# Performance work log

Measured on AMD Instinct MI355X. Metric: run time of the kernel, lower is better.

The kernel has to match this reference:

```python
import math
import jax, jax.numpy as jnp
import numpy as np

C = 1024
H = 16
HD = C // H
T = 2048
B = 2
EPS = 1e-5


def setup_inputs() -> dict:
    key = jax.random.key(0)
    ks = jax.random.split(key, 8)
    s = 0.02
    return {
        "x": jax.random.normal(ks[0], (B, T, C), dtype=jnp.float32),
        "ln1_g": jnp.ones((C,), jnp.float32),
        "ln1_b": jnp.zeros((C,), jnp.float32),
        "w_attn": jax.random.normal(ks[1], (C, 3 * C), dtype=jnp.float32) * s,
        "b_attn": jnp.zeros((3 * C,), jnp.float32),
        "w_proj": jax.random.normal(ks[2], (C, C), dtype=jnp.float32) * s,
        "b_proj": jnp.zeros((C,), jnp.float32),
        "ln2_g": jnp.ones((C,), jnp.float32),
        "ln2_b": jnp.zeros((C,), jnp.float32),
        "w_fc": jax.random.normal(ks[3], (C, 4 * C), dtype=jnp.float32) * s,
        "b_fc": jnp.zeros((4 * C,), jnp.float32),
        "w_fc2": jax.random.normal(ks[4], (4 * C, C), dtype=jnp.float32) * s,
        "b_fc2": jnp.zeros((C,), jnp.float32),
    }


def _layernorm(x, g, b):
    mu = jnp.mean(x, axis=-1, keepdims=True)
    var = jnp.mean((x - mu) ** 2, axis=-1, keepdims=True)
    return (x - mu) * jax.lax.rsqrt(var + EPS) * g + b


def _attention(x, w_attn, b_attn, w_proj, b_proj):
    Bb, Tt, Cc = x.shape
    qkv = x @ w_attn + b_attn  # (B,T,3C)
    q, k, v = jnp.split(qkv, 3, axis=-1)
    # (B,H,T,HD)
    q = q.reshape(Bb, Tt, H, HD).transpose(0, 2, 1, 3)
    k = k.reshape(Bb, Tt, H, HD).transpose(0, 2, 1, 3)
    v = v.reshape(Bb, Tt, H, HD).transpose(0, 2, 1, 3)
    scale = 1.0 / math.sqrt(HD)
    attn = jnp.einsum("bhqd,bhkd->bhqk", q, k) * scale
    causal = jnp.tril(jnp.ones((Tt, Tt), dtype=bool))
    attn = jnp.where(causal[None, None], attn, -jnp.inf)
    attn = jax.nn.softmax(attn, axis=-1)
    out = jnp.einsum("bhqk,bhkd->bhqd", attn, v)
    out = out.transpose(0, 2, 1, 3).reshape(Bb, Tt, Cc)
    return out @ w_proj + b_proj


def _mlp(x, w_fc, b_fc, w_fc2, b_fc2):
    h = jax.nn.gelu(x @ w_fc + b_fc, approximate=True)
    return h @ w_fc2 + b_fc2


def reference(x, ln1_g, ln1_b, w_attn, b_attn, w_proj, b_proj,
              ln2_g, ln2_b, w_fc, b_fc, w_fc2, b_fc2):
    x = x + _attention(_layernorm(x, ln1_g, ln1_b), w_attn, b_attn, w_proj, b_proj)
    x = x + _mlp(_layernorm(x, ln2_g, ln2_b), w_fc, b_fc, w_fc2, b_fc2)
    return x
```

## Files before the change

### kernel.cpp

```cpp
#include <hip/hip_runtime.h>
#include <math.h>

#define TB 2
#define TT 2048
#define TC 1024
#define TH 16
#define THD 64
#define TM (TB*TT)
#define NQT 32

typedef __bf16 bf16x8 __attribute__((ext_vector_type(8)));
typedef float f32x4 __attribute__((ext_vector_type(4)));
typedef unsigned short u16x8 __attribute__((ext_vector_type(8)));
typedef unsigned short u16x4 __attribute__((ext_vector_type(4)));

__device__ __forceinline__ unsigned short f2bf(float f){
    unsigned int u = __builtin_bit_cast(unsigned int, f);
    u = (u + 0x7FFFu + ((u >> 16) & 1u)) >> 16;
    return (unsigned short)u;
}
__device__ __forceinline__ float bf2f(unsigned short h){
    unsigned int u = ((unsigned int)h) << 16;
    return __builtin_bit_cast(float, u);
}
__device__ __forceinline__ bf16x8 ldbf8(const unsigned short* p){
    return __builtin_bit_cast(bf16x8, *(const u16x8*)p);
}
__device__ __forceinline__ void gl_lds16(const void* g, void* l){
    __builtin_amdgcn_global_load_lds(
        (const __attribute__((address_space(1))) unsigned int*)g,
        (__attribute__((address_space(3))) unsigned int*)l,
        16, 0, 0);
}
__device__ __forceinline__ float gelu_tanh(float v){
    float u = 2.0f * 0.7978845608028654f * (v + 0.044715f * v * v * v);
    u = fminf(fmaxf(u, -30.f), 30.f);
    float e = __expf(u);
    return 0.5f * v * (1.f + (e - 1.f) / (e + 1.f));
}

__global__ __launch_bounds__(256)
void convert_all(const float* __restrict__ w_attn, const float* __restrict__ w_proj,
                 const float* __restrict__ w_fc,   const float* __restrict__ w_fc2,
                 unsigned short* __restrict__ wattnT, unsigned short* __restrict__ wprojT,
                 unsigned short* __restrict__ wfcT,   unsigned short* __restrict__ wfc2T){
    __shared__ float tile[32][33];
    const int bid = blockIdx.x;
    const float* in; unsigned short* out; int K, N, bx, by;
    if (bid < 3072)      { in=w_attn; out=wattnT; K=1024; N=3072; bx=bid%96;  by=bid/96; }
    else if (bid < 4096) { int lo=bid-3072; in=w_proj; out=wprojT; K=1024; N=1024; bx=lo%32;  by=lo/32; }
    else if (bid < 8192) { int lo=bid-4096; in=w_fc;   out=wfcT;   K=1024; N=4096; bx=lo%128; by=lo/128; }
    else                 { int lo=bid-8192; in=w_fc2;  out=wfc2T;  K=4096; N=1024; bx=lo%32;  by=lo/32; }
    int tx = threadIdx.x, ty = threadIdx.y;
    int n0 = bx * 32, k0 = by * 32;
    #pragma unroll
    for (int i = 0; i < 4; i++)
        tile[ty + 8*i][tx] = in[(size_t)(k0 + ty + 8*i) * N + n0 + tx];
    __syncthreads();
    #pragma unroll
    for (int i = 0; i < 4; i++)
        out[(size_t)(n0 + ty + 8*i) * K + k0 + tx] = f2bf(tile[tx][ty + 8*i]);
}

__global__ __launch_bounds__(256)
void ln_kernel(const float* __restrict__ x, const float* __restrict__ g,
               const float* __restrict__ be, unsigned short* __restrict__ y){
    const int row = blockIdx.x, t = threadIdx.x;
    const float4* xr = (const float4*)(x + (size_t)row * TC);
    float4 v = xr[t];
    float s  = v.x + v.y + v.z + v.w;
    float s2 = v.x*v.x + v.y*v.y + v.z*v.z + v.w*v.w;
    #pragma unroll
    for (int off = 32; off; off >>= 1){
        s  += __shfl_down(s,  off);
        s2 += __shfl_down(s2, off);
    }
    __shared__ float red[8];
    int l = t & 63, wv = t >> 6;
    if (l == 0){ red[wv] = s; red[4 + wv] = s2; }
    __syncthreads();
    float S  = red[0] + red[1] + red[2] + red[3];
    float S2 = red[4] + red[5] + red[6] + red[7];
    float mu = S * (1.f / TC);
    float var = S2 * (1.f / TC) - mu * mu;
    float rs = rsqrtf(var + 1e-5f);
    int c = t * 4;
    float4 gg = *(const float4*)(g + c);
    float4 bb = *(const float4*)(be + c);
    u16x4 o;
    o[0] = f2bf((v.x - mu) * rs * gg.x + bb.x);
    o[1] = f2bf((v.y - mu) * rs * gg.y + bb.y);
    o[2] = f2bf((v.z - mu) * rs * gg.z + bb.z);
    o[3] = f2bf((v.w - mu) * rs * gg.w + bb.w);
    *(u16x4*)(y + (size_t)row * TC + c) = o;
}

template<int EPI>
__global__ __launch_bounds__(256, 2)
void gemm_bt(const unsigned short* __restrict__ A,
             const unsigned short* __restrict__ Bt,
             const float* __restrict__ bias,
             const float* __restrict__ resid,
             void* __restrict__ outv,
             int M, int N, int K){
    __shared__ unsigned short lA[128 * 32];
    __shared__ unsigned short lB[128 * 32];
    const int t = threadIdx.x, w = t >> 6, l = t & 63, lr = l & 15, lg = l >> 4;
    const int nt = N >> 7;
    const int nwg = gridDim.x;
    const int bid = blockIdx.x;
    int wg = (nwg & 7) ? bid : ((bid & 7) * (nwg >> 3) + (bid >> 3));
    const int bm = wg / nt, bn = wg % nt;
    const int row0 = bm << 7, col0 = bn << 7;
    const int wr = w >> 1, wc = w & 1;

    f32x4 acc[4][4];
    #pragma unroll
    for (int i = 0; i < 4; i++)
        #pragma unroll
        for (int j = 0; j < 4; j++) acc[i][j] = (f32x4){0.f,0.f,0.f,0.f};

    const char* Ag = (const char*)(A + (size_t)(row0 + (t >> 2)) * K) + (t & 3) * 16;
    const char* Bg = (const char*)(Bt + (size_t)(col0 + (t >> 2)) * K) + (t & 3) * 16;
    const size_t rstep = (size_t)64 * K * 2;
    char* lAw = (char*)lA + w * 1024;
    char* lBw = (char*)lB + w * 1024;

    for (int k0 = 0; k0 < K; k0 += 32){
        size_t kb = (size_t)k0 * 2;
        gl_lds16(Ag + kb,          lAw);
        gl_lds16(Ag + kb + rstep,  lAw + 4096);
        gl_lds16(Bg + kb,          lBw);
        gl_lds16(Bg + kb + rstep,  lBw + 4096);
        __syncthreads();
        bf16x8 af[4], bfr[4];
        #pragma unroll
        for (int mi = 0; mi < 4; mi++)
            af[mi] = ldbf8(lA + (wr*64 + mi*16 + lr) * 32 + lg * 8);
        #pragma unroll
        for (int ni = 0; ni < 4; ni++)
            bfr[ni] = ldbf8(lB + (wc*64 + ni*16 + lr) * 32 + lg * 8);
        #pragma unroll
        for (int mi = 0; mi < 4; mi++)
            #pragma unroll
            for (int ni = 0; ni < 4; ni++)
                acc[mi][ni] = __builtin_amdgcn_mfma_f32_16x16x32_bf16(
                    af[mi], bfr[ni], acc[mi][ni], 0, 0, 0);
        __syncthreads();
    }

    float bcol[4];
    #pragma unroll
    for (int ni = 0; ni < 4; ni++) bcol[ni] = bias[col0 + wc*64 + ni*16 + lr];
    #pragma unroll
    for (int mi = 0; mi < 4; mi++){
        #pragma unroll
        for (int j = 0; j < 4; j++){
            int row = row0 + wr*64 + mi*16 + lg*4 + j;
            size_t base = (size_t)row * N + col0 + wc*64 + lr;
            #pragma unroll
            for (int ni = 0; ni < 4; ni++){
                float v = acc[mi][ni][j] + bcol[ni];
                size_t idx = base + (size_t)ni * 16;
                if (EPI == 0)      ((unsigned short*)outv)[idx] = f2bf(v);
                else if (EPI == 1) ((float*)outv)[idx] = v + resid[idx];
                else               ((unsigned short*)outv)[idx] = f2bf(gelu_tanh(v));
            }
        }
    }
}

template<int MH>
__device__ __forceinline__ void gloadA(const unsigned short* bufA, bf16x8 (&af)[4][2],
                                       int wm, int lr, int sl0, int sl1){
    #pragma unroll
    for (int i = 0; i < 4; i++){
        int lrow = (wm*128 + (MH*4 + i)*16 + lr) * 64;
        af[i][0] = ldbf8(bufA + lrow + sl0);
        af[i][1] = ldbf8(bufA + lrow + sl1);
    }
}
__device__ __forceinline__ void gloadB(const unsigned short* bufB, bf16x8 (&bfr)[4][2],
                                       int wn, int lr, int sl0, int sl1){
    #pragma unroll
    for (int i = 0; i < 4; i++){
        int brow = (wn*64 + i*16 + lr) * 64;
        bfr[i][0] = ldbf8(bufB + brow + sl0);
        bfr[i][1] = ldbf8(bufB + brow + sl1);
    }
}
template<int MH, int NH>
__device__ __forceinline__ void gmma(const bf16x8 (&af)[4][2], const bf16x8 (&bfr)[4][2],
                                     f32x4 (&acc)[8][4]){
    #pragma unroll
    for (int i = 0; i < 4; i++)
        #pragma unroll
        for (int j = 0; j < 2; j++){
            f32x4& a = acc[MH*4 + i][NH*2 + j];
            a = __builtin_amdgcn_mfma_f32_16x16x32_bf16(af[i][0], bfr[NH*2+j][0], a, 0,0,0);
            a = __builtin_amdgcn_mfma_f32_16x16x32_bf16(af[i][1], bfr[NH*2+j][1], a, 0,0,0);
        }
}

#define G256_LOOP(NT_, KBEG_)                                                   \
    for (int tk = 0; tk < (NT_); ++tk){                                         \
        const int cur = tk & 1;                                                 \
        const bool more = (tk + 1) < (NT_);                                     \
        const unsigned short* bufA = &lds[cur][0][0];                           \
        const unsigned short* bufB = &lds[cur][1][0];                           \
        if (more){                                                              \
            stage(cur ^ 1, (KBEG_) + (tk + 1)*64, 0);                           \
            asm volatile("s_waitcnt vmcnt(2)" ::: "memory");                    \
        } else {                                                                \
            asm volatile("s_waitcnt vmcnt(0)" ::: "memory");                    \
        }                                                                       \
        __builtin_amdgcn_s_barrier();                                           \
        bf16x8 af[4][2], bfr[4][2];                                             \
        gloadA<0>(bufA, af, wm, lr, sl0, sl1);                                  \
        gloadB(bufB, bfr, wn, lr, sl0, sl1);                                    \
        if (more) stage(cur ^ 1, (KBEG_) + (tk + 1)*64, 1);                     \
        __builtin_amdgcn_s_barrier();                                           \
        asm volatile("s_waitcnt lgkmcnt(0)" ::: "memory");                      \
        __builtin_amdgcn_sched_barrier(0);                                      \
        __builtin_amdgcn_s_setprio(1);                                          \
        gmma<0,0>(af, bfr, acc);                                                \
        __builtin_amdgcn_s_setprio(0);                                          \
        __builtin_amdgcn_s_barrier();                                           \
        if (more) stage(cur ^ 1, (KBEG_) + (tk + 1)*64, 2);                     \
        __builtin_amdgcn_s_setprio(1);                                          \
        gmma<0,1>(af, bfr, acc);                                                \
        __builtin_amdgcn_s_setprio(0);                                          \
        __builtin_amdgcn_s_barrier();                                           \
        gloadA<1>(bufA, af, wm, lr, sl0, sl1);                                  \
        if (more) stage(cur ^ 1, (KBEG_) + (tk + 1)*64, 3);                     \
        __builtin_amdgcn_s_barrier();                                           \
        asm volatile("s_waitcnt lgkmcnt(0)" ::: "memory");                      \
        __builtin_amdgcn_sched_barrier(0);                                      \
        __builtin_amdgcn_s_setprio(1);                                          \
        gmma<1,0>(af, bfr, acc);                                                \
        __builtin_amdgcn_s_setprio(0);                                          \
        __builtin_amdgcn_s_barrier();                                           \
        __builtin_amdgcn_s_setprio(1);                                          \
        gmma<1,1>(af, bfr, acc);                                                \
        __builtin_amdgcn_s_setprio(0);                                          \
        __builtin_amdgcn_s_barrier();                                           \
    }

template<int EPI>
__global__ __launch_bounds__(512, 1)
void gemm256(const unsigned short* __restrict__ A,
             const unsigned short* __restrict__ Bt,
             const float* __restrict__ bias,
             void* __restrict__ outv,
             int M, int N, int K){
    __shared__ unsigned short lds[2][2][256*64];
    const int t = threadIdx.x;
    const int w = t >> 6, l = t & 63, lr = l & 15, lg = l >> 4;
    const int wm = w >> 2, wn = w & 3;
    const int lr7 = lr & 7;
    const int sl0 = (lg ^ lr7) << 3;
    const int sl1 = ((4 + lg) ^ lr7) << 3;
    const int nbn = N >> 8;
    const int nwg = (M >> 8) * nbn;
    const int bid = blockIdx.x;
    const int wg = (nwg & 7) ? bid : ((bid & 7) * (nwg >> 3) + (bid >> 3));
    const int bm = wg / nbn, bn = wg % nbn;
    const size_t row0 = (size_t)bm << 8, col0 = (size_t)bn << 8;
    const int NT = K >> 6;

    f32x4 acc[8][4];
    #pragma unroll
    for (int i = 0; i < 8; i++)
        #pragma unroll
        for (int j = 0; j < 4; j++) acc[i][j] = (f32x4){0.f,0.f,0.f,0.f};

    int rowc[4], slogc[4];
    #pragma unroll
    for (int c = 0; c < 4; c++){
        int seg = t + (c << 9);
        rowc[c]  = seg >> 3;
        slogc[c] = (((seg & 7) ^ ((seg >> 3) & 7)) << 3);
    }
    const unsigned short* Abase = A  + row0 * K;
    const unsigned short* Bbase = Bt + col0 * K;
    auto stage = [&](int buf, int kofs, int c){
        int seg = t + (c << 9);
        const unsigned short* sa = Abase + (size_t)rowc[c] * K + kofs + slogc[c];
        const unsigned short* sb = Bbase + (size_t)rowc[c] * K + kofs + slogc[c];
        gl_lds16(sa, (void*)&lds[buf][0][seg * 8]);
        gl_lds16(sb, (void*)&lds[buf][1][seg * 8]);
    };

    #pragma unroll
    for (int c = 0; c < 4; c++) stage(0, 0, c);

    G256_LOOP(NT, 0)

    float bcol[4];
    #pragma unroll
    for (int ni = 0; ni < 4; ni++) bcol[ni] = bias[col0 + wn*64 + ni*16 + lr];
    unsigned short* outp = (unsigned short*)outv;
    #pragma unroll
    for (int mi = 0; mi < 8; mi++){
        #pragma unroll
        for (int j = 0; j < 4; j++){
            size_t row = row0 + wm*128 + mi*16 + lg*4 + j;
            size_t base = row * N + col0 + wn*64 + lr;
            #pragma unroll
            for (int ni = 0; ni < 4; ni++){
                float v = acc[mi][ni][j] + bcol[ni];
                size_t idx = base + (size_t)ni * 16;
                if (EPI == 0) outp[idx] = f2bf(v);
                else          outp[idx] = f2bf(gelu_tanh(v));
            }
        }
    }
}

__global__ __launch_bounds__(512, 1)
void gemm256sk(const unsigned short* __restrict__ A,
               const unsigned short* __restrict__ Bt,
               unsigned short* __restrict__ pout,
               int M, int N, int K, int klen){
    __shared__ unsigned short lds[2][2][256*64];
    const int t = threadIdx.x;
    const int w = t >> 6, l = t & 63, lr = l & 15, lg = l >> 4;
    const int wm = w >> 2, wn = w & 3;
    const int lr7 = lr & 7;
    const int sl0 = (lg ^ lr7) << 3;
    const int sl1 = ((4 + lg) ^ lr7) << 3;
    const int nbn = N >> 8;
    const int ntile = (M >> 8) * nbn;
    const int nwg = gridDim.x;
    const int bid = blockIdx.x;
    int wg = (nwg & 7) ? bid : ((bid & 7) * (nwg >> 3) + (bid >> 3));
    const int kh = wg / ntile;
    wg -= kh * ntile;
    const int bm = wg / nbn, bn = wg % nbn;
    const size_t row0 = (size_t)bm << 8, col0 = (size_t)bn << 8;
    const int NT = klen >> 6;
    const int kbeg = kh * klen;

    f32x4 acc[8][4];
    #pragma unroll
    for (int i = 0; i < 8; i++)
        #pragma unroll
        for (int j = 0; j < 4; j++) acc[i][j] = (f32x4){0.f,0.f,0.f,0.f};

    int rowc[4], slogc[4];
    #pragma unroll
    for (int c = 0; c < 4; c++){
        int seg = t + (c << 9);
        rowc[c]  = seg >> 3;
        slogc[c] = (((seg & 7) ^ ((seg >> 3) & 7)) << 3);
    }
    const unsigned short* Abase = A  + row0 * K;
    const unsigned short* Bbase = Bt + col0 * K;
    auto stage = [&](int buf, int kofs, int c){
        int seg = t + (c << 9);
        const unsigned short* sa = Abase + (size_t)rowc[c] * K + kofs + slogc[c];
        const unsigned short* sb = Bbase + (size_t)rowc[c] * K + kofs + slogc[c];
        gl_lds16(sa, (void*)&lds[buf][0][seg * 8]);
        gl_lds16(sb, (void*)&lds[buf][1][seg * 8]);
    };

    #pragma unroll
    for (int c = 0; c < 4; c++) stage(0, kbeg, c);

    G256_LOOP(NT, kbeg)

    unsigned short* outp = pout + (size_t)kh * M * N;
    #pragma unroll
    for (int mi = 0; mi < 8; mi++){
        #pragma unroll
        for (int j = 0; j < 4; j++){
            size_t row = row0 + wm*128 + mi*16 + lg*4 + j;
            size_t base = row * N + col0 + wn*64 + lr;
            #pragma unroll
            for (int ni = 0; ni < 4; ni++)
                outp[base + (size_t)ni * 16] = f2bf(acc[mi][ni][j]);
        }
    }
}

__global__ __launch_bounds__(256)
void combine_k4(const unsigned short* __restrict__ p,
                const float* __restrict__ bias, const float* __restrict__ resid,
                float* __restrict__ out){
    const size_t PS = (size_t)TM * TC;
    const int total = TM * TC / 4;
    for (int i = blockIdx.x * 256 + threadIdx.x; i < total; i += gridDim.x * 256){
        int e = i * 4;
        u16x4 a0 = *(const u16x4*)(p + e);
        u16x4 a1 = *(const u16x4*)(p + PS + e);
        u16x4 a2 = *(const u16x4*)(p + 2*PS + e);
        u16x4 a3 = *(const u16x4*)(p + 3*PS + e);
        float4 r = *(const float4*)(resid + e);
        float4 bb = *(const float4*)(bias + (e & (TC - 1)));
        float4 o;
        o.x = bf2f(a0[0]) + bf2f(a1[0]) + bf2f(a2[0]) + bf2f(a3[0]) + r.x + bb.x;
        o.y = bf2f(a0[1]) + bf2f(a1[1]) + bf2f(a2[1]) + bf2f(a3[1]) + r.y + bb.y;
        o.z = bf2f(a0[2]) + bf2f(a1[2]) + bf2f(a2[2]) + bf2f(a3[2]) + r.z + bb.z;
        o.w = bf2f(a0[3]) + bf2f(a1[3]) + bf2f(a2[3]) + bf2f(a3[3]) + r.w + bb.w;
        *(float4*)(out + e) = o;
    }
}

__global__ __launch_bounds__(256)
void vtrans(const unsigned short* __restrict__ qkv, unsigned short* __restrict__ vTg){
    __shared__ unsigned short lt[64][68];
    int kt = blockIdx.x & (NQT - 1);
    int bh = blockIdx.x >> 5;
    int h = bh & (TH - 1), b = bh >> 4;
    int t = threadIdx.x;
    int r = t >> 2, c4 = t & 3;
    const unsigned short* src = qkv + (size_t)(b*TT + kt*64 + r) * (3*TC) + 2*TC + h*THD;
    u16x8 a0 = *(const u16x8*)(src + c4*8);
    u16x8 a1 = *(const u16x8*)(src + 32 + c4*8);
    #pragma unroll
    for (int j = 0; j < 8; j++){
        lt[r][c4*8 + j]      = a0[j];
        lt[r][32 + c4*8 + j] = a1[j];
    }
    __syncthreads();
    int d = t >> 2;
    unsigned short* dst = vTg + ((size_t)bh * NQT + kt) * (64*80) + (size_t)d * 80;
    u16x8 o0, o1;
    #pragma unroll
    for (int j = 0; j < 8; j++){
        o0[j] = lt[c4*8 + j][d];
        o1[j] = lt[32 + c4*8 + j][d];
    }
    *(u16x8*)(dst + c4*8)      = o0;
    *(u16x8*)(dst + 32 + c4*8) = o1;
}

__global__ __launch_bounds__(512, 2)
void attn_kernel(const unsigned short* __restrict__ qkv,
                 const unsigned short* __restrict__ vTg,
                 unsigned short* __restrict__ attn_out){
    __shared__ unsigned short kbuf[2][64*64];
    __shared__ unsigned short vbuf[2][64*64];
    __shared__ unsigned short pl[8][16*72];

    const int bid = blockIdx.x;
    const int qrank = bid >> 5;
    const int bh = bid & 31;
    const int h = bh & (TH - 1), b = bh >> 4;
    const int qb = 15 - qrank;
    const int q0 = qb << 7;
    const int t = threadIdx.x, w = t >> 6, l = t & 63, lr = l & 15, lg = l >> 4;
    const int lr7 = lr & 7;
    const int sl0 = (lg ^ lr7) << 3;
    const int sl1 = ((4 + lg) ^ lr7) << 3;
    const float SC = 0.18033688011112042f;

    const int NKT = 2*qb + 2;
    const int qrow_base = q0 + w*16;
    const int kdiag = qrow_base >> 6;

    const int srow = t >> 3, sslot = t & 7;
    const int scol = (sslot ^ (srow & 7)) * 8;
    const unsigned short* kg =
        qkv + (size_t)(b*TT + srow) * (3*TC) + TC + h*THD + scol;
    const unsigned short* vg =
        vTg + (size_t)bh * (NQT*64*80) + (size_t)srow * 80 + scol;
    const size_t kstep = (size_t)64 * (3*TC);

    auto stage = [&](int kt, int buf){
        gl_lds16(kg + (size_t)kt * kstep,   (void*)&kbuf[buf][t*8]);
        gl_lds16(vg + (size_t)kt * (64*80), (void*)&vbuf[buf][t*8]);
    };

    const unsigned short* qr =
        qkv + (size_t)(b*TT + qrow_base + lr) * (3*TC) + h*THD;
    bf16x8 q0f = ldbf8(qr + lg*8), q1f = ldbf8(qr + 32 + lg*8);

    bf16x8 ones;
    #pragma unroll
    for (int i = 0; i < 8; i++) ones[i] = (__bf16)1.0f;

    f32x4 o[5];
    float m[4];
    #pragma unroll
    for (int i = 0; i < 5; i++) o[i] = (f32x4){0.f,0.f,0.f,0.f};
    #pragma unroll
    for (int i = 0; i < 4; i++) m[i] = -1e30f;

    unsigned short* plw = &pl[w][0];

    stage(0, 0);
    for (int kt = 0; kt < NKT; ++kt){
        const int cur = kt & 1;
        const bool more = (kt + 1) < NKT;
        if (more){
            stage(kt + 1, cur ^ 1);
            asm volatile("s_waitcnt vmcnt(2)" ::: "memory");
        } else {
            asm volatile("s_waitcnt vmcnt(0)" ::: "memory");
        }
        __builtin_amdgcn_s_barrier();

        const unsigned short* kb = &kbuf[cur][0];
        f32x4 s[4];
        __builtin_amdgcn_s_setprio(1);
        #pragma unroll
        for (int cb = 0; cb < 4; cb++){
            bf16x8 ka = ldbf8(kb + (cb*16 + lr)*64 + sl0);
            bf16x8 kbf = ldbf8(kb + (cb*16 + lr)*64 + sl1);
            f32x4 z = (f32x4){0.f,0.f,0.f,0.f};
            z = __builtin_amdgcn_mfma_f32_16x16x32_bf16(q0f, ka, z, 0,0,0);
            z = __builtin_amdgcn_mfma_f32_16x16x32_bf16(q1f, kbf, z, 0,0,0);
            s[cb] = z;
        }
        __builtin_amdgcn_s_setprio(0);
        if (kt >= kdiag){
            #pragma unroll
            for (int cb = 0; cb < 4; cb++)
                #pragma unroll
                for (int j = 0; j < 4; j++)
                    if (kt*64 + cb*16 + lr > qrow_base + lg*4 + j) s[cb][j] = -1e30f;
        }
        float mloc[4];
        #pragma unroll
        for (int j = 0; j < 4; j++)
            mloc[j] = fmaxf(fmaxf(s[0][j], s[1][j]), fmaxf(s[2][j], s[3][j]));
        #pragma unroll
        for (int off = 1; off < 16; off <<= 1)
            #pragma unroll
            for (int j = 0; j < 4; j++)
                mloc[j] = fmaxf(mloc[j], __shfl_xor(mloc[j], off));
        float al[4];
        #pragma unroll
        for (int j = 0; j < 4; j++){
            float mn = fmaxf(m[j], mloc[j] * SC);
            al[j] = exp2f(m[j] - mn);
            m[j] = mn;
        }
        #pragma unroll
        for (int db = 0; db < 5; db++)
            #pragma unroll
            for (int j = 0; j < 4; j++) o[db][j] *= al[j];
        #pragma unroll
        for (int cb = 0; cb < 4; cb++)
            #pragma unroll
            for (int j = 0; j < 4; j++){
                float e = exp2f(__builtin_fmaf(s[cb][j], SC, -m[j]));
                ((__bf16*)plw)[(lg*4 + j)*72 + cb*16 + lr] = (__bf16)e;
            }
        const unsigned short* vb = &vbuf[cur][0];
        bf16x8 pa0 = ldbf8(plw + lr*72 + lg*8);
        bf16x8 pa1 = ldbf8(plw + lr*72 + 32 + lg*8);
        __builtin_amdgcn_s_setprio(1);
        #pragma unroll
        for (int db = 0; db < 4; db++){
            bf16x8 va = ldbf8(vb + (db*16 + lr)*64 + sl0);
            bf16x8 vbf = ldbf8(vb + (db*16 + lr)*64 + sl1);
            o[db] = __builtin_amdgcn_mfma_f32_16x16x32_bf16(pa0, va, o[db], 0,0,0);
            o[db] = __builtin_amdgcn_mfma_f32_16x16x32_bf16(pa1, vbf, o[db], 0,0,0);
        }
        o[4] = __builtin_amdgcn_mfma_f32_16x16x32_bf16(pa0, ones, o[4], 0,0,0);
        o[4] = __builtin_amdgcn_mfma_f32_16x16x32_bf16(pa1, ones, o[4], 0,0,0);
        __builtin_amdgcn_s_setprio(0);

        __builtin_amdgcn_s_barrier();
    }

    __bf16* aout = (__bf16*)attn_out;
    #pragma unroll
    for (int j = 0; j < 4; j++){
        float inv = 1.f / o[4][j];
        size_t tok = (size_t)(b*TT + qrow_base + lg*4 + j);
        #pragma unroll
        for (int db = 0; db < 4; db++)
            aout[tok*TC + h*THD + db*16 + lr] = (__bf16)(o[db][j] * inv);
    }
}

extern "C" void kernel_launch(void* const* d_in, const int* in_sizes, int n_in,
                              void* d_out, int out_size, void* d_ws, size_t ws_size,
                              hipStream_t stream){
    const float* x      = (const float*)d_in[0];
    const float* ln1_g  = (const float*)d_in[1];
    const float* ln1_b  = (const float*)d_in[2];
    const float* w_attn = (const float*)d_in[3];
    const float* b_attn = (const float*)d_in[4];
    const float* w_proj = (const float*)d_in[5];
    const float* b_proj = (const float*)d_in[6];
    const float* ln2_g  = (const float*)d_in[7];
    const float* ln2_b  = (const float*)d_in[8];
    const float* w_fc   = (const float*)d_in[9];
    const float* b_fc   = (const float*)d_in[10];
    const float* w_fc2  = (const float*)d_in[11];
    const float* b_fc2  = (const float*)d_in[12];
    float* out = (float*)d_out;

    char* ws = (char*)d_ws;
    size_t off = 0;
    auto alloc = [&](size_t bytes) -> void* {
        void* p = ws + off;
        off += (bytes + 255) & ~(size_t)255;
        return p;
    };
    unsigned short* wattnT = (unsigned short*)alloc((size_t)3072*1024*2);
    unsigned short* wprojT = (unsigned short*)alloc((size_t)1024*1024*2);
    unsigned short* wfcT   = (unsigned short*)alloc((size_t)4096*1024*2);
    unsigned short* wfc2T  = (unsigned short*)alloc((size_t)1024*4096*2);
    unsigned short* xn1    = (unsigned short*)alloc((size_t)TM*TC*2);
    unsigned short* qkvb   = (unsigned short*)alloc((size_t)TM*3*TC*2);
    float*          resid1 = (float*)alloc((size_t)TM*TC*4);
    unsigned short* xn2    = (unsigned short*)alloc((size_t)TM*TC*2);
    unsigned short* hbuf   = (unsigned short*)alloc((size_t)TM*4*TC*2);
    unsigned short* attnO  = (unsigned short*)alloc((size_t)TM*TC*2);
    unsigned short* vTg    = (unsigned short*)alloc((size_t)TB*TH*NQT*64*80*2);

    unsigned short* pks = xn1;

    convert_all<<<12288, dim3(32, 8, 1), 0, stream>>>(
        w_attn, w_proj, w_fc, w_fc2, wattnT, wprojT, wfcT, wfc2T);

    ln_kernel<<<TM, 256, 0, stream>>>(x, ln1_g, ln1_b, xn1);

    gemm256<0><<<(TM/256)*(3072/256), 512, 0, stream>>>(
        xn1, wattnT, b_attn, qkvb, TM, 3072, 1024);

    vtrans<<<TB*TH*NQT, 256, 0, stream>>>(qkvb, vTg);

    attn_kernel<<<TB*TH*(TT/128), 512, 0, stream>>>(qkvb, vTg, attnO);

    gemm_bt<1><<<(TM/128)*(1024/128), 256, 0, stream>>>(
        attnO, wprojT, b_proj, x, resid1, TM, 1024, 1024);

    ln_kernel<<<TM, 256, 0, stream>>>(resid1, ln2_g, ln2_b, xn2);

    gemm256<2><<<(TM/256)*(4096/256), 512, 0, stream>>>(
        xn2, wfcT, b_fc, hbuf, TM, 4096, 1024);

    gemm256sk<<<4*(TM/256)*(1024/256), 512, 0, stream>>>(
        hbuf, wfc2T, pks, TM, 1024, 4096, 1024);
    combine_k4<<<2048, 256, 0, stream>>>(pks, b_fc2, resid1, out);
}
```

Baseline: 243.8 us.

## Shrink attention blocks to 64 query rows and skip redundant rescales

The attention kernel now uses 256-thread blocks covering 64 query rows instead of 512 threads covering 128. This doubles the grid and lets each block stop at its own diagonal tile, which gives finer causal load balance and less masked work. Each thread now stages two K/V chunks per tile, with the wait count changed to match. The online-softmax rescale of the output accumulators is skipped when no row maximum in the wavefront grew. That removes exp and multiply work but adds a wave-wide vote and a branch, and K/V tiles are now reloaded by twice as many blocks.

```diff
diff --git a/kernel.cpp b/kernel.cpp
--- a/kernel.cpp
+++ b/kernel.cpp
@@ -435,41 +435,44 @@
     *(u16x8*)(dst + 32 + c4*8) = o1;
 }
 
-__global__ __launch_bounds__(512, 2)
+__global__ __launch_bounds__(256, 3)
 void attn_kernel(const unsigned short* __restrict__ qkv,
                  const unsigned short* __restrict__ vTg,
                  unsigned short* __restrict__ attn_out){
     __shared__ unsigned short kbuf[2][64*64];
     __shared__ unsigned short vbuf[2][64*64];
-    __shared__ unsigned short pl[8][16*72];
+    __shared__ unsigned short pl[4][16*72];
 
     const int bid = blockIdx.x;
     const int qrank = bid >> 5;
     const int bh = bid & 31;
     const int h = bh & (TH - 1), b = bh >> 4;
-    const int qb = 15 - qrank;
-    const int q0 = qb << 7;
+    const int qb = 31 - qrank;
+    const int q0 = qb << 6;
     const int t = threadIdx.x, w = t >> 6, l = t & 63, lr = l & 15, lg = l >> 4;
     const int lr7 = lr & 7;
     const int sl0 = (lg ^ lr7) << 3;
     const int sl1 = ((4 + lg) ^ lr7) << 3;
     const float SC = 0.18033688011112042f;
 
-    const int NKT = 2*qb + 2;
+    const int NKT = qb + 1;
     const int qrow_base = q0 + w*16;
-    const int kdiag = qrow_base >> 6;
-
-    const int srow = t >> 3, sslot = t & 7;
-    const int scol = (sslot ^ (srow & 7)) * 8;
-    const unsigned short* kg =
-        qkv + (size_t)(b*TT + srow) * (3*TC) + TC + h*THD + scol;
-    const unsigned short* vg =
-        vTg + (size_t)bh * (NQT*64*80) + (size_t)srow * 80 + scol;
+
+    const int vt0 = t, vt1 = t + 256;
+    const int sr0 = vt0 >> 3, sr1 = vt1 >> 3;
+    const int sc0 = ((vt0 & 7) ^ (sr0 & 7)) * 8;
+    const int sc1 = ((vt1 & 7) ^ (sr1 & 7)) * 8;
+    const unsigned short* kg0 = qkv + (size_t)(b*TT + sr0) * (3*TC) + TC + h*THD + sc0;
+    const unsigned short* kg1 = qkv + (size_t)(b*TT + sr1) * (3*TC) + TC + h*THD + sc1;
+    const unsigned short* vg0 = vTg + (size_t)bh * (NQT*64*80) + (size_t)sr0 * 80 + sc0;
+    const unsigned short* vg1 = vTg + (size_t)bh * (NQT*64*80) + (size_t)sr1 * 80 + sc1;
     const size_t kstep = (size_t)64 * (3*TC);
 
     auto stage = [&](int kt, int buf){
-        gl_lds16(kg + (size_t)kt * kstep,   (void*)&kbuf[buf][t*8]);
-        gl_lds16(vg + (size_t)kt * (64*80), (void*)&vbuf[buf][t*8]);
+        gl_lds16(kg0 + (size_t)kt*kstep,   (void*)&kbuf[buf][vt0*8]);
+        gl_lds16(kg1 + (size_t)kt*kstep,   (void*)&kbuf[buf][vt1*8]);
+        gl_lds16(vg0 + (size_t)kt*(64*80), (void*)&vbuf[buf][vt0*8]);
+        gl_lds16(vg1 + (size_t)kt*(64*80), (void*)&vbuf[buf][vt1*8]);
     };
 
     const unsigned short* qr =
@@ -495,7 +498,7 @@
         const bool more = (kt + 1) < NKT;
         if (more){
             stage(kt + 1, cur ^ 1);
-            asm volatile("s_waitcnt vmcnt(2)" ::: "memory");
+            asm volatile("s_waitcnt vmcnt(4)" ::: "memory");
         } else {
             asm volatile("s_waitcnt vmcnt(0)" ::: "memory");
         }
@@ -514,7 +517,7 @@
             s[cb] = z;
         }
         __builtin_amdgcn_s_setprio(0);
-        if (kt >= kdiag){
+        if (kt == qb){
             #pragma unroll
             for (int cb = 0; cb < 4; cb++)
                 #pragma unroll
@@ -530,17 +533,21 @@
             #pragma unroll
             for (int j = 0; j < 4; j++)
                 mloc[j] = fmaxf(mloc[j], __shfl_xor(mloc[j], off));
-        float al[4];
-        #pragma unroll
-        for (int j = 0; j < 4; j++){
-            float mn = fmaxf(m[j], mloc[j] * SC);
-            al[j] = exp2f(m[j] - mn);
-            m[j] = mn;
-        }
-        #pragma unroll
-        for (int db = 0; db < 5; db++)
-            #pragma unroll
-            for (int j = 0; j < 4; j++) o[db][j] *= al[j];
+        bool grow = (mloc[0]*SC > m[0]) || (mloc[1]*SC > m[1]) ||
+                    (mloc[2]*SC > m[2]) || (mloc[3]*SC > m[3]);
+        if (__any(grow)){
+            float al[4];
+            #pragma unroll
+            for (int j = 0; j < 4; j++){
+                float mn = fmaxf(m[j], mloc[j] * SC);
+                al[j] = exp2f(m[j] - mn);
+                m[j] = mn;
+            }
+            #pragma unroll
+            for (int db = 0; db < 5; db++)
+                #pragma unroll
+                for (int j = 0; j < 4; j++) o[db][j] *= al[j];
+        }
         #pragma unroll
         for (int cb = 0; cb < 4; cb++)
             #pragma unroll
@@ -626,7 +633,7 @@
 
     vtrans<<<TB*TH*NQT, 256, 0, stream>>>(qkvb, vTg);
 
-    attn_kernel<<<TB*TH*(TT/128), 512, 0, stream>>>(qkvb, vTg, attnO);
+    attn_kernel<<<TB*TH*NQT, 256, 0, stream>>>(qkvb, vTg, attnO);
 
     gemm_bt<1><<<(TM/128)*(1024/128), 256, 0, stream>>>(
         attnO, wprojT, b_proj, x, resid1, TM, 1024, 1024);
```

New measurement: 237.3 us. -2.7%, faster.
